# Kernel optimization log

Measured on AMD Instinct MI355X. Metric: run time of the kernel, lower is better.

## Reference

```python
import jax, jax.numpy as jnp
import numpy as np
from jax import lax

T_D = 0.7          # condensation radius
T_B = 0.2          # min beta to seed a condensate
FEATURE_LENGTH = 9 # columns of raw features before the prediction block
N_FEAT = 17        # n_ccoords = N_FEAT - 14 = 3
N_EVENTS = 16
POINTS_PER_EVENT = 65536


def setup_inputs() -> dict:
    key = jax.random.key(0)
    N = N_EVENTS * POINTS_PER_EVENT
    # uniform [0,1): betas in [0,1), ccoords in the unit cube -> realistic clustering
    x = jax.random.uniform(key, (N, N_FEAT), dtype=jnp.float32)
    row_splits = (jnp.arange(N_EVENTS + 1) * POINTS_PER_EVENT).astype(jnp.int32)
    return {"x": x, "row_splits": row_splits}


def _build_condensates(ccoords, betas, radius, min_beta):
    """Greedy NMS-like condensation, vectorized over events.
    ccoords: [E, P, C] float; betas: [E, P] float.
    Returns asso [E,P] int32 (index of assigned condensate, -1 = noise) and
    iscond [E,P] bool (condensation point flags).
    """
    E, P, _ = ccoords.shape
    r2 = radius * radius

    def masked_beta(asso):
        return jnp.where(asso < 0, betas, -1.0)

    def cond_fn(state):
        asso, _ = state
        return jnp.any(jnp.max(masked_beta(asso), axis=1) >= min_beta)

    def body_fn(state):
        asso, iscond = state
        mb = masked_beta(asso)                     # [E,P]
        ref = jnp.argmax(mb, axis=1)               # [E] highest-beta unassigned point
        valid = jnp.take_along_axis(mb, ref[:, None], axis=1)[:, 0] >= min_beta  # [E]
        refc = jnp.take_along_axis(ccoords, ref[:, None, None], axis=1)          # [E,1,C]
        distsq = jnp.sum((ccoords - refc) ** 2, axis=-1)                          # [E,P]
        assign = (asso < 0) & (distsq <= r2) & valid[:, None]
        asso = jnp.where(assign, ref[:, None].astype(jnp.int32), asso)
        newcond = (jnp.arange(P)[None, :] == ref[:, None]) & valid[:, None]
        return asso, iscond | newcond

    asso0 = jnp.full((E, P), -1, dtype=jnp.int32)
    iscond0 = jnp.zeros((E, P), dtype=jnp.bool_)
    return lax.while_loop(cond_fn, body_fn, (asso0, iscond0))


def reference(x, row_splits):
    E = row_splits.shape[0] - 1
    N, F = x.shape
    P = N // E  # uniform events (RaggedConstructTensor equivalent for equal splits)
    n_ccoords = F - 14
    x_pred = x[:, FEATURE_LENGTH:]
    n_pred = x_pred.shape[-1]
    betas = x_pred[:, 0].reshape(E, P)
    ccoords = x_pred[:, n_pred - n_ccoords:].reshape(E, P, n_ccoords)

    asso, iscond = _build_condensates(ccoords, betas, T_D, T_B)

    ncond = jnp.sum(iscond, axis=1).astype(jnp.int32)  # condensates per event
    out_row_splits = jnp.concatenate(
        [jnp.zeros((1,), jnp.int32), jnp.cumsum(ncond).astype(jnp.int32)])
    # jit-safe equivalent of dout = x[iscond > 0]: zero-mask non-condensates
    mask = iscond.reshape(-1, 1).astype(x.dtype)
    dout = x * mask  # [N, F], rows of non-condensates are zero
    return dout, out_row_splits
```

## Files before the change

kernel.cpp:

```cpp
#include <hip/hip_runtime.h>

typedef unsigned long long u64;
typedef unsigned int u32;

static constexpr int NF = 17;
static constexpr int BCOL = 9;
static constexpr int CCOL = 14;
static constexpr int CONDCAP = 256;
static constexpr int NPASS = 4;
static constexpr int RPB = 512;
static constexpr int MAXIT = 8;

#define T_B_F ((float)0.2)
#define R2_F  ((float)(0.7*0.7))

__device__ __forceinline__ u64 kmax(u64 a, u64 b){ return a > b ? a : b; }

__device__ __forceinline__ u64 shfl_down_u64(u64 v, int off){
    u32 lo = (u32)v, hi = (u32)(v >> 32);
    lo = __shfl_down(lo, off, 64);
    hi = __shfl_down(hi, off, 64);
    return ((u64)hi << 32) | lo;
}

__device__ __forceinline__ u64 waveReduceMax(u64 k){
    #pragma unroll
    for (int off = 32; off > 0; off >>= 1){
        u64 o = shfl_down_u64(k, off);
        if (o > k) k = o;
    }
    return k;
}

__device__ __forceinline__ float dist2(float cx, float cy, float cz,
                                       float rx, float ry, float rz){
    #pragma clang fp contract(off)
    float dx = cx - rx, dy = cy - ry, dz = cz - rz;
    float sx = dx * dx, sy = dy * dy, sz = dz * dz;
    return (sx + sy) + sz;
}

__device__ __forceinline__ u64 makeKey(float beta, u32 idx){
    return ((u64)__float_as_uint(beta) << 32) | (u64)(0xFFFFFFFFu - idx);
}

__global__ void k_init(u32* ws){
    int t = threadIdx.x;
    if (t < 1024) ws[t] = 0;
}

__global__ __launch_bounds__(256) void k_filter(
    const float4* __restrict__ x4, float4* __restrict__ out4,
    u64* __restrict__ argmax0, int* __restrict__ cnt0,
    float4* __restrict__ cA, int* __restrict__ iA,
    int P, int chunksPerEvent)
{
    __shared__ float lds[RPB * NF];
    __shared__ int swc[4], swb[4], sbase;
    __shared__ u64 sred[4];

    int e = blockIdx.x / chunksPerEvent;
    int chunk = blockIdx.x % chunksPerEvent;
    int rowStart = chunk * RPB;
    size_t tile4 = (size_t)blockIdx.x * (RPB * NF / 4);

    float4* lds4 = (float4*)lds;
    const int N4 = RPB * NF / 4;
    float4 z = make_float4(0.f, 0.f, 0.f, 0.f);
    for (int i = threadIdx.x; i < N4; i += 256){
        lds4[i] = x4[tile4 + i];
        out4[tile4 + i] = z;
    }
    __syncthreads();

    int tid = threadIdx.x, lid = tid & 63, wid = tid >> 6;
    int r0 = tid, r1 = tid + 256;
    float be0 = lds[r0*NF+BCOL], cx0 = lds[r0*NF+CCOL], cy0 = lds[r0*NF+CCOL+1], cz0 = lds[r0*NF+CCOL+2];
    float be1 = lds[r1*NF+BCOL], cx1 = lds[r1*NF+CCOL], cy1 = lds[r1*NF+CCOL+1], cz1 = lds[r1*NF+CCOL+2];
    bool k0 = (be0 >= T_B_F), k1 = (be1 >= T_B_F);
    u64 bal0 = __ballot(k0), bal1 = __ballot(k1);
    int wcnt = __popcll(bal0) + __popcll(bal1);

    u64 lk = 0;
    if (k0) lk = makeKey(be0, (u32)(rowStart + r0));
    if (k1) lk = kmax(lk, makeKey(be1, (u32)(rowStart + r1)));
    u64 kw = waveReduceMax(lk);
    if (lid == 0){ swc[wid] = wcnt; sred[wid] = kw; }
    __syncthreads();
    if (tid == 0){
        int tot = 0;
        for (int w = 0; w < 4; w++){ swb[w] = tot; tot += swc[w]; }
        sbase = tot ? atomicAdd(&cnt0[e], tot) : 0;
        u64 m = sred[0];
        for (int i = 1; i < 4; i++) m = kmax(m, sred[i]);
        if (m) atomicMax(&argmax0[e], m);
    }
    __syncthreads();
    int base = sbase + swb[wid];
    u64 lm = (1ull << lid) - 1;
    size_t eoff = (size_t)e * P;
    if (k0){
        int pos = base + __popcll(bal0 & lm);
        cA[eoff + pos] = make_float4(cx0, cy0, cz0, be0);
        iA[eoff + pos] = rowStart + r0;
    }
    if (k1){
        int pos = base + __popcll(bal0) + __popcll(bal1 & lm);
        cA[eoff + pos] = make_float4(cx1, cy1, cz1, be1);
        iA[eoff + pos] = rowStart + r1;
    }
}

__global__ __launch_bounds__(256) void k_pass(
    const float* __restrict__ x,
    const float4* __restrict__ cIn, const int* __restrict__ iIn,
    float4* __restrict__ cOut, int* __restrict__ iOut,
    const u64* __restrict__ argmaxIn, u64* __restrict__ argmaxOut,
    const int* __restrict__ cntIn, int* __restrict__ cntOut,
    int* __restrict__ ncond, int* __restrict__ condlist,
    int P, int blocksPerEvent)
{
    __shared__ int swc[4], swb[4], sbase;
    __shared__ u64 sred[4];

    int e = blockIdx.x / blocksPerEvent;
    int c = blockIdx.x % blocksPerEvent;
    u64 key = argmaxIn[e];
    float betaRef = __uint_as_float((u32)(key >> 32));
    if (!(betaRef >= T_B_F)) return;
    u32 refIdx = 0xFFFFFFFFu - (u32)(key & 0xFFFFFFFFu);
    if (c == 0 && threadIdx.x == 0){
        int s = atomicAdd(&ncond[e], 1);
        if (s < CONDCAP) condlist[e * CONDCAP + s] = (int)refIdx;
    }
    size_t rbase = ((size_t)e * P + refIdx) * NF;
    float rx = x[rbase + CCOL], ry = x[rbase + CCOL + 1], rz = x[rbase + CCOL + 2];

    int n = cntIn[e];
    int tid = threadIdx.x, lid = tid & 63, wid = tid >> 6;
    size_t eoff = (size_t)e * P;
    int stride = blocksPerEvent * 256;

    float4 cc[MAXIT]; int ix[MAXIT]; bool kp[MAXIT]; u64 bal[MAXIT];
    int wcnt = 0;
    u64 lk = 0;
    #pragma unroll
    for (int k = 0; k < MAXIT; k++){
        int i = c * 256 + tid + k * stride;
        bool inb = i < n;
        int ii = inb ? i : 0;
        cc[k] = cIn[eoff + ii];
        ix[k] = iIn[eoff + ii];
        float d2 = dist2(cc[k].x, cc[k].y, cc[k].z, rx, ry, rz);
        kp[k] = inb && !(d2 <= R2_F);
        bal[k] = __ballot(kp[k]);
        wcnt += __popcll(bal[k]);
        if (kp[k]) lk = kmax(lk, makeKey(cc[k].w, (u32)ix[k]));
    }
    u64 kw = waveReduceMax(lk);
    if (lid == 0){ swc[wid] = wcnt; sred[wid] = kw; }
    __syncthreads();
    if (tid == 0){
        int tot = 0;
        for (int w = 0; w < 4; w++){ swb[w] = tot; tot += swc[w]; }
        sbase = tot ? atomicAdd(&cntOut[e], tot) : 0;
        u64 m = sred[0];
        for (int i = 1; i < 4; i++) m = kmax(m, sred[i]);
        if (m) atomicMax(&argmaxOut[e], m);
    }
    __syncthreads();
    int pos = sbase + swb[wid];
    u64 lm = (1ull << lid) - 1;
    #pragma unroll
    for (int k = 0; k < MAXIT; k++){
        if (kp[k]){
            int p_ = pos + __popcll(bal[k] & lm);
            cOut[eoff + p_] = cc[k];
            iOut[eoff + p_] = ix[k];
        }
        pos += __popcll(bal[k]);
    }
}

__global__ __launch_bounds__(1024) void k_finish(
    const float* __restrict__ x,
    float4* cA, int* iA, float4* cB, int* iB,
    const u64* __restrict__ argmax2, const int* __restrict__ cnt2,
    int* __restrict__ ncond, int* __restrict__ condlist, int P)
{
    int e = blockIdx.x;
    __shared__ u64 sred[16];
    __shared__ int scnt;
    __shared__ u64 skey;
    __shared__ float srefc[3];

    int n = cnt2[e];
    u64 key = argmax2[e];
    float4* cIn = cA + (size_t)e * P; int* iIn = iA + (size_t)e * P;
    float4* cOut = cB + (size_t)e * P; int* iOut = iB + (size_t)e * P;
    int tid = threadIdx.x, lid = tid & 63, wid = tid >> 6;

    while (true){
        float betaRef = __uint_as_float((u32)(key >> 32));
        if (!(betaRef >= T_B_F)) break;
        u32 refIdx = 0xFFFFFFFFu - (u32)(key & 0xFFFFFFFFu);
        if (tid == 0){
            int s = atomicAdd(&ncond[e], 1);
            if (s < CONDCAP) condlist[e * CONDCAP + s] = (int)refIdx;
            size_t rbase = ((size_t)e * P + refIdx) * NF;
            srefc[0] = x[rbase + CCOL];
            srefc[1] = x[rbase + CCOL + 1];
            srefc[2] = x[rbase + CCOL + 2];
            scnt = 0;
        }
        __syncthreads();
        float rx = srefc[0], ry = srefc[1], rz = srefc[2];
        u64 localKey = 0;
        for (int i = tid; i < n; i += 1024){
            float4 cc = cIn[i]; int idx = iIn[i];
            float d2 = dist2(cc.x, cc.y, cc.z, rx, ry, rz);
            bool keep = !(d2 <= R2_F);
            u64 bal = __ballot(keep);
            int cw = __popcll(bal);
            int b_ = 0;
            if (lid == 0) b_ = cw ? atomicAdd(&scnt, cw) : 0;
            b_ = __shfl(b_, 0, 64);
            if (keep){
                int pos = b_ + __popcll(bal & ((1ull << lid) - 1));
                cOut[pos] = cc; iOut[pos] = idx;
                localKey = kmax(localKey, makeKey(cc.w, (u32)idx));
            }
        }
        u64 kw = waveReduceMax(localKey);
        if (lid == 0) sred[wid] = kw;
        __syncthreads();
        if (tid == 0){
            u64 m = 0;
            for (int i = 0; i < 16; i++) m = kmax(m, sred[i]);
            skey = m;
        }
        __syncthreads();
        key = skey;
        n = scnt;
        { float4* t = cIn; cIn = cOut; cOut = t; }
        { int* t = iIn; iIn = iOut; iOut = t; }
        __syncthreads();
    }
}

__global__ void k_out(const float* __restrict__ x, float* __restrict__ out,
                      const int* __restrict__ ncond, const int* __restrict__ condlist,
                      int P, int E)
{
    int e = blockIdx.x;
    if (e == 0 && threadIdx.x < E + 1){
        int s = 0;
        for (int i = 0; i < (int)threadIdx.x; i++) s += ncond[i];
        out[(size_t)E * P * NF + threadIdx.x] = (float)s;
    }
    int nc = ncond[e];
    if (nc > CONDCAP) nc = CONDCAP;
    int tot = nc * NF;
    for (int i = threadIdx.x; i < tot; i += blockDim.x){
        int j = i / NF, f = i - j * NF;
        int row = condlist[e * CONDCAP + j];
        size_t base = ((size_t)e * P + row) * NF;
        out[base + f] = x[base + f];
    }
}

extern "C" void kernel_launch(void* const* d_in, const int* in_sizes, int n_in,
                              void* d_out, int out_size, void* d_ws, size_t ws_size,
                              hipStream_t stream) {
    const float* x = (const float*)d_in[0];
    int N = in_sizes[0] / NF;
    int E = in_sizes[1] - 1;
    int P = N / E;
    float* out = (float*)d_out;
    char* ws = (char*)d_ws;

    u64* argmax = (u64*)ws;
    int* cnt    = (int*)(ws + 1024);
    int* ncond  = (int*)(ws + 2048);
    int* condlist = (int*)(ws + 4096);
    size_t listOff = 32768;
    size_t listElems = (size_t)E * P;
    float4* cA = (float4*)(ws + listOff);
    float4* cB = (float4*)(ws + listOff + listElems * 16);
    int* iA = (int*)(ws + listOff + listElems * 32);
    int* iB = (int*)(ws + listOff + listElems * 36);

    k_init<<<1, 1024, 0, stream>>>((u32*)ws);

    int chunksPerEvent = P / RPB;
    k_filter<<<E * chunksPerEvent, 256, 0, stream>>>(
        (const float4*)x, (float4*)out, argmax, cnt, cA, iA, P, chunksPerEvent);

    int bpe = 32;
    float4* cs[2] = {cA, cB};
    int* is[2] = {iA, iB};
    for (int r = 0; r < NPASS; r++){
        k_pass<<<E * bpe, 256, 0, stream>>>(
            x, cs[r & 1], is[r & 1], cs[(r + 1) & 1], is[(r + 1) & 1],
            argmax + r * E, argmax + (r + 1) * E,
            cnt + r * E, cnt + (r + 1) * E,
            ncond, condlist, P, bpe);
    }

    k_finish<<<E, 1024, 0, stream>>>(
        x, cA, iA, cB, iB, argmax + NPASS * E, cnt + NPASS * E, ncond, condlist, P);

    k_out<<<E, 256, 0, stream>>>(x, out, ncond, condlist, P, E);
}
```

Before: 193.3 us.

## Shrink filter LDS, carry argmax payload, batch finish loop, fuse output kernel

The filter kernel now keeps only the beta and cluster-coordinate columns of each row in a compact float4 LDS array instead of staging the full 17-column tile. The per-event finish loop processes CHK candidates per thread with one atomic per wave per chunk, and carries the winning candidate's coordinates through the reduction so the reference point is not re-read from global memory each iteration. The separate output-copy kernel is folded into the finish kernel, with a last-block counter writing the row splits. Parallel passes drop from four to two, which leaves more serial work to the single-block-per-event finish loop.

Measured after the change: 207.1 us. 1.07x slower.

```diff
diff --git a/kernel.cpp b/kernel.cpp
--- a/kernel.cpp
+++ b/kernel.cpp
@@ -7,9 +7,10 @@
 static constexpr int BCOL = 9;
 static constexpr int CCOL = 14;
 static constexpr int CONDCAP = 256;
-static constexpr int NPASS = 4;
+static constexpr int NPASS = 2;
 static constexpr int RPB = 512;
 static constexpr int MAXIT = 8;
+static constexpr int CHK = 8;
 
 #define T_B_F ((float)0.2)
 #define R2_F  ((float)(0.7*0.7))
@@ -55,7 +56,7 @@
     float4* __restrict__ cA, int* __restrict__ iA,
     int P, int chunksPerEvent)
 {
-    __shared__ float lds[RPB * NF];
+    __shared__ float4 lrow[RPB];
     __shared__ int swc[4], swb[4], sbase;
     __shared__ u64 sred[4];
 
@@ -64,26 +65,33 @@
     int rowStart = chunk * RPB;
     size_t tile4 = (size_t)blockIdx.x * (RPB * NF / 4);
 
-    float4* lds4 = (float4*)lds;
     const int N4 = RPB * NF / 4;
     float4 z = make_float4(0.f, 0.f, 0.f, 0.f);
     for (int i = threadIdx.x; i < N4; i += 256){
-        lds4[i] = x4[tile4 + i];
+        float4 v = x4[tile4 + i];
         out4[tile4 + i] = z;
+        float vv[4] = {v.x, v.y, v.z, v.w};
+        int f0 = 4 * i;
+        #pragma unroll
+        for (int j = 0; j < 4; j++){
+            int flat = f0 + j;
+            int row = flat / NF;
+            int col = flat - row * NF;
+            if (col == BCOL)       ((float*)&lrow[row])[3] = vv[j];
+            else if (col >= CCOL)  ((float*)&lrow[row])[col - CCOL] = vv[j];
+        }
     }
     __syncthreads();
 
     int tid = threadIdx.x, lid = tid & 63, wid = tid >> 6;
-    int r0 = tid, r1 = tid + 256;
-    float be0 = lds[r0*NF+BCOL], cx0 = lds[r0*NF+CCOL], cy0 = lds[r0*NF+CCOL+1], cz0 = lds[r0*NF+CCOL+2];
-    float be1 = lds[r1*NF+BCOL], cx1 = lds[r1*NF+CCOL], cy1 = lds[r1*NF+CCOL+1], cz1 = lds[r1*NF+CCOL+2];
-    bool k0 = (be0 >= T_B_F), k1 = (be1 >= T_B_F);
+    float4 a0 = lrow[tid], a1 = lrow[tid + 256];
+    bool k0 = (a0.w >= T_B_F), k1 = (a1.w >= T_B_F);
     u64 bal0 = __ballot(k0), bal1 = __ballot(k1);
     int wcnt = __popcll(bal0) + __popcll(bal1);
 
     u64 lk = 0;
-    if (k0) lk = makeKey(be0, (u32)(rowStart + r0));
-    if (k1) lk = kmax(lk, makeKey(be1, (u32)(rowStart + r1)));
+    if (k0) lk = makeKey(a0.w, (u32)(rowStart + tid));
+    if (k1) lk = kmax(lk, makeKey(a1.w, (u32)(rowStart + tid + 256)));
     u64 kw = waveReduceMax(lk);
     if (lid == 0){ swc[wid] = wcnt; sred[wid] = kw; }
     __syncthreads();
@@ -101,13 +109,13 @@
     size_t eoff = (size_t)e * P;
     if (k0){
         int pos = base + __popcll(bal0 & lm);
-        cA[eoff + pos] = make_float4(cx0, cy0, cz0, be0);
-        iA[eoff + pos] = rowStart + r0;
+        cA[eoff + pos] = a0;
+        iA[eoff + pos] = rowStart + tid;
     }
     if (k1){
         int pos = base + __popcll(bal0) + __popcll(bal1 & lm);
-        cA[eoff + pos] = make_float4(cx1, cy1, cz1, be1);
-        iA[eoff + pos] = rowStart + r1;
+        cA[eoff + pos] = a1;
+        iA[eoff + pos] = rowStart + tid + 256;
     }
 }
 
@@ -183,22 +191,25 @@
 }
 
 __global__ __launch_bounds__(1024) void k_finish(
-    const float* __restrict__ x,
+    const float* __restrict__ x, float* __restrict__ out,
     float4* cA, int* iA, float4* cB, int* iB,
-    const u64* __restrict__ argmax2, const int* __restrict__ cnt2,
-    int* __restrict__ ncond, int* __restrict__ condlist, int P)
+    const u64* __restrict__ argmaxN, const int* __restrict__ cntN,
+    int* __restrict__ ncond, int* __restrict__ condlist,
+    int* __restrict__ done, int P, int E)
 {
     int e = blockIdx.x;
-    __shared__ u64 sred[16];
-    __shared__ int scnt;
+    __shared__ u64 skey16[16];
+    __shared__ float4 spay16[16];
+    __shared__ int scnt, sNC, sLast;
     __shared__ u64 skey;
     __shared__ float srefc[3];
 
-    int n = cnt2[e];
-    u64 key = argmax2[e];
+    int tid = threadIdx.x, lid = tid & 63, wid = tid >> 6;
+    int n = cntN[e];
+    u64 key = argmaxN[e];
     float4* cIn = cA + (size_t)e * P; int* iIn = iA + (size_t)e * P;
     float4* cOut = cB + (size_t)e * P; int* iOut = iB + (size_t)e * P;
-    int tid = threadIdx.x, lid = tid & 63, wid = tid >> 6;
+    bool havePay = false;
 
     while (true){
         float betaRef = __uint_as_float((u32)(key >> 32));
@@ -207,37 +218,68 @@
         if (tid == 0){
             int s = atomicAdd(&ncond[e], 1);
             if (s < CONDCAP) condlist[e * CONDCAP + s] = (int)refIdx;
-            size_t rbase = ((size_t)e * P + refIdx) * NF;
-            srefc[0] = x[rbase + CCOL];
-            srefc[1] = x[rbase + CCOL + 1];
-            srefc[2] = x[rbase + CCOL + 2];
+            if (!havePay){
+                size_t rb = ((size_t)e * P + refIdx) * NF;
+                srefc[0] = x[rb + CCOL];
+                srefc[1] = x[rb + CCOL + 1];
+                srefc[2] = x[rb + CCOL + 2];
+            }
             scnt = 0;
         }
+        havePay = true;
         __syncthreads();
         float rx = srefc[0], ry = srefc[1], rz = srefc[2];
-        u64 localKey = 0;
-        for (int i = tid; i < n; i += 1024){
-            float4 cc = cIn[i]; int idx = iIn[i];
-            float d2 = dist2(cc.x, cc.y, cc.z, rx, ry, rz);
-            bool keep = !(d2 <= R2_F);
-            u64 bal = __ballot(keep);
-            int cw = __popcll(bal);
-            int b_ = 0;
-            if (lid == 0) b_ = cw ? atomicAdd(&scnt, cw) : 0;
-            b_ = __shfl(b_, 0, 64);
-            if (keep){
-                int pos = b_ + __popcll(bal & ((1ull << lid) - 1));
-                cOut[pos] = cc; iOut[pos] = idx;
-                localKey = kmax(localKey, makeKey(cc.w, (u32)idx));
+
+        u64 bk = 0; float bx = 0.f, by = 0.f, bz = 0.f;
+        for (int base = 0; base < n; base += 1024 * CHK){
+            float4 cc[CHK]; int ix[CHK]; bool kp[CHK]; u64 bal[CHK];
+            int wcnt = 0;
+            #pragma unroll
+            for (int k = 0; k < CHK; k++){
+                int i = base + k * 1024 + tid;
+                bool inb = i < n;
+                int ii = inb ? i : 0;
+                cc[k] = cIn[ii];
+                ix[k] = iIn[ii];
+                float d2 = dist2(cc[k].x, cc[k].y, cc[k].z, rx, ry, rz);
+                kp[k] = inb && !(d2 <= R2_F);
+                bal[k] = __ballot(kp[k]);
+                wcnt += __popcll(bal[k]);
+                if (kp[k]){
+                    u64 mk = makeKey(cc[k].w, (u32)ix[k]);
+                    if (mk > bk){ bk = mk; bx = cc[k].x; by = cc[k].y; bz = cc[k].z; }
+                }
             }
-        }
-        u64 kw = waveReduceMax(localKey);
-        if (lid == 0) sred[wid] = kw;
+            int wbase = 0;
+            if (lid == 0) wbase = wcnt ? atomicAdd(&scnt, wcnt) : 0;
+            wbase = __shfl(wbase, 0, 64);
+            u64 lm = (1ull << lid) - 1;
+            #pragma unroll
+            for (int k = 0; k < CHK; k++){
+                if (kp[k]){
+                    int p_ = wbase + __popcll(bal[k] & lm);
+                    cOut[p_] = cc[k];
+                    iOut[p_] = ix[k];
+                }
+                wbase += __popcll(bal[k]);
+            }
+        }
+        #pragma unroll
+        for (int off = 32; off > 0; off >>= 1){
+            u64 ok = shfl_down_u64(bk, off);
+            float ox = __shfl_down(bx, off, 64);
+            float oy = __shfl_down(by, off, 64);
+            float oz = __shfl_down(bz, off, 64);
+            if (ok > bk){ bk = ok; bx = ox; by = oy; bz = oz; }
+        }
+        if (lid == 0){ skey16[wid] = bk; spay16[wid] = make_float4(bx, by, bz, 0.f); }
         __syncthreads();
         if (tid == 0){
-            u64 m = 0;
-            for (int i = 0; i < 16; i++) m = kmax(m, sred[i]);
+            u64 m = 0; float4 pp = make_float4(0.f, 0.f, 0.f, 0.f);
+            for (int i = 0; i < 16; i++)
+                if (skey16[i] > m){ m = skey16[i]; pp = spay16[i]; }
             skey = m;
+            srefc[0] = pp.x; srefc[1] = pp.y; srefc[2] = pp.z;
         }
         __syncthreads();
         key = skey;
@@ -246,26 +288,28 @@
         { int* t = iIn; iIn = iOut; iOut = t; }
         __syncthreads();
     }
-}
-
-__global__ void k_out(const float* __restrict__ x, float* __restrict__ out,
-                      const int* __restrict__ ncond, const int* __restrict__ condlist,
-                      int P, int E)
-{
-    int e = blockIdx.x;
-    if (e == 0 && threadIdx.x < E + 1){
-        int s = 0;
-        for (int i = 0; i < (int)threadIdx.x; i++) s += ncond[i];
-        out[(size_t)E * P * NF + threadIdx.x] = (float)s;
-    }
-    int nc = ncond[e];
-    if (nc > CONDCAP) nc = CONDCAP;
-    int tot = nc * NF;
-    for (int i = threadIdx.x; i < tot; i += blockDim.x){
+
+    if (tid == 0) sNC = atomicAdd(&ncond[e], 0);
+    __syncthreads();
+    int nc = sNC; if (nc > CONDCAP) nc = CONDCAP;
+    for (int i = tid; i < nc * NF; i += 1024){
         int j = i / NF, f = i - j * NF;
         int row = condlist[e * CONDCAP + j];
-        size_t base = ((size_t)e * P + row) * NF;
-        out[base + f] = x[base + f];
+        size_t b = ((size_t)e * P + row) * NF;
+        out[b + f] = x[b + f];
+    }
+
+    __threadfence();
+    if (tid == 0) sLast = atomicAdd(done, 1);
+    __syncthreads();
+    if (sLast == E - 1 && tid == 0){
+        size_t so = (size_t)E * P * NF;
+        int s = 0;
+        out[so] = 0.f;
+        for (int i = 0; i < E; i++){
+            s += atomicAdd(&ncond[i], 0);
+            out[so + i + 1] = (float)s;
+        }
     }
 }
 
@@ -282,6 +326,7 @@
     u64* argmax = (u64*)ws;
     int* cnt    = (int*)(ws + 1024);
     int* ncond  = (int*)(ws + 2048);
+    int* done   = (int*)(ws + 2560);
     int* condlist = (int*)(ws + 4096);
     size_t listOff = 32768;
     size_t listElems = (size_t)E * P;
@@ -308,7 +353,6 @@
     }
 
     k_finish<<<E, 1024, 0, stream>>>(
-        x, cA, iA, cB, iB, argmax + NPASS * E, cnt + NPASS * E, ncond, condlist, P);
-
-    k_out<<<E, 256, 0, stream>>>(x, out, ncond, condlist, P, E);
-}
+        x, out, cA, iA, cB, iB, argmax + NPASS * E, cnt + NPASS * E,
+        ncond, condlist, done, P, E);
+}
```
